# Optimization experiments

Measured on AMD Instinct MI355X. Metric: run time of the kernel, lower is better.

Reference implementation:

```python
import jax, jax.numpy as jnp
import numpy as np

B, N, L, K, C1 = 128, 300, 600, 19, 100  # batch, num_cnns, input_length, filter_size, fc hidden
PS = 7  # pool size == stride
LC = L - (K - 1)               # 582, conv output length
LP = (LC - PS) // PS + 1       # 83, pooled length
NC = 2                         # num_classes
EPS = 1e-5


def _bn(x, g, b, m, v):
    # eval-mode batchnorm, params broadcast along given axes already
    return g * (x - m) * jax.lax.rsqrt(v + EPS) + b


def setup_inputs() -> dict:
    key = jax.random.key(0)
    ks = jax.random.split(key, 20)
    f = lambda i, shape, s=0.1: (jax.random.normal(ks[i], shape, dtype=jnp.float32) * s)
    pv = lambda i, shape: (jax.random.uniform(ks[i], shape, dtype=jnp.float32) + 0.5)
    return {
        'x': jax.random.normal(ks[0], (B, 4, L), dtype=jnp.float32),
        'conv_w': f(1, (N, 4, K)), 'conv_b': f(2, (N,)),
        'bn1_g': pv(3, (N,)), 'bn1_b': f(4, (N,)), 'bn1_m': f(5, (N,)), 'bn1_v': pv(6, (N,)),
        'fc1_w': f(7, (N, C1, LP)), 'fc1_b': f(8, (N, C1)),
        'bn2_g': pv(9, (N, C1)), 'bn2_b': f(10, (N, C1)), 'bn2_m': f(11, (N, C1)), 'bn2_v': pv(12, (N, C1)),
        'fc2_w': f(13, (N, C1)), 'fc2_b': f(14, (N,)),
        'bn3_g': pv(15, (N,)), 'bn3_b': f(16, (N,)), 'bn3_m': f(17, (N,)), 'bn3_v': pv(18, (N,)),
        'final_w': f(19, (NC, N)), 'final_b': jnp.zeros((NC,), dtype=jnp.float32),
    }


def reference(x, conv_w, conv_b, bn1_g, bn1_b, bn1_m, bn1_v,
              fc1_w, fc1_b, bn2_g, bn2_b, bn2_m, bn2_v,
              fc2_w, fc2_b, bn3_g, bn3_b, bn3_m, bn3_v,
              final_w, final_b):
    # grouped conv on a repeated input == plain conv with 4 in-channels, N out-channels
    h = jax.lax.conv_general_dilated(x, conv_w, window_strides=(1,), padding='VALID',
                                     dimension_numbers=('NCH', 'OIH', 'NCH'))  # [B,N,582]
    h = h + conv_b[None, :, None]
    h = _bn(h, bn1_g[None, :, None], bn1_b[None, :, None], bn1_m[None, :, None], bn1_v[None, :, None])
    h = jnp.exp(h)
    # MaxPool1d(7,7): [B,N,582] -> [B,N,83]
    h = jax.lax.reduce_window(h, -jnp.inf, jax.lax.max,
                              window_dimensions=(1, 1, PS), window_strides=(1, 1, PS), padding='VALID')
    # grouped 1x1 conv == per-unit dense: [B,N,83] x [N,100,83] -> [B,N,100]
    h = jnp.einsum('bnp,nhp->bnh', h, fc1_w) + fc1_b[None]
    h = jax.nn.relu(_bn(h, bn2_g[None], bn2_b[None], bn2_m[None], bn2_v[None]))
    # second grouped 1x1 conv: [B,N,100] x [N,100] -> [B,N]
    h = jnp.einsum('bnh,nh->bn', h, fc2_w) + fc2_b[None]
    h = jax.nn.relu(_bn(h, bn3_g[None], bn3_b[None], bn3_m[None], bn3_v[None]))
    return h @ final_w.T + final_b  # [B,num_classes]
```

## Files before the change

kernel.cpp:

```cpp
#include <hip/hip_runtime.h>
#include <math.h>

#define EPS_ 1e-5f

__global__ __launch_bounds__(256) void kP(const float* __restrict__ conv_w,
                                          float* __restrict__ cw4) {
    const int cq = blockIdx.x;
    const int c  = cq / 5;
    const int kq = cq - c * 5;
    for (int n = threadIdx.x; n < 300; n += 256) {
        float4 v;
        const int k0 = 4 * kq;
        v.x = (k0 + 0 < 19) ? conv_w[n * 76 + c * 19 + k0 + 0] : 0.f;
        v.y = (k0 + 1 < 19) ? conv_w[n * 76 + c * 19 + k0 + 1] : 0.f;
        v.z = (k0 + 2 < 19) ? conv_w[n * 76 + c * 19 + k0 + 2] : 0.f;
        v.w = (k0 + 3 < 19) ? conv_w[n * 76 + c * 19 + k0 + 3] : 0.f;
        reinterpret_cast<float4*>(cw4)[(c * 5 + kq) * 300 + n] = v;
    }
}

__global__ __launch_bounds__(64) void kA(
        const float* __restrict__ x,
        const float* __restrict__ cw4,
        const float* __restrict__ conv_b,
        const float* __restrict__ g1, const float* __restrict__ b1,
        const float* __restrict__ m1, const float* __restrict__ v1,
        float* __restrict__ pooled)
{
    const int id  = blockIdx.x;
    const int b   = id / 112;
    const int sub = id - b * 112;
    if (sub >= 105) return;
    const int ng  = sub / 21;
    const int pc  = sub - ng * 21;
    const int p0c = pc * 4;
    const int p0  = (p0c > 79) ? 79 : p0c;
    const int lane = threadIdx.x;
    const int n   = ng * 64 + lane;
    const int nc  = (n < 300) ? n : 299;

    const float4* w4 = reinterpret_cast<const float4*>(cw4);

    float acc[28];
    #pragma unroll
    for (int i = 0; i < 28; ++i) acc[i] = 0.f;

    #pragma unroll 1
    for (int c = 0; c < 4; ++c) {
        const float* xc = x + b * 2400 + c * 600 + 7 * p0;
        float xw[46];
        #pragma unroll
        for (int j = 0; j < 46; ++j) xw[j] = xc[j];
        #pragma unroll
        for (int kq = 0; kq < 5; ++kq) {
            const float4 wv = w4[(c * 5 + kq) * 300 + nc];
            const int ni = (kq == 4) ? 3 : 4;
            #pragma unroll
            for (int i = 0; i < ni; ++i) {
                const int k = 4 * kq + i;
                const float wvv = (i == 0) ? wv.x : (i == 1) ? wv.y
                                : (i == 2) ? wv.z : wv.w;
                #pragma unroll
                for (int p = 0; p < 4; ++p)
                    #pragma unroll
                    for (int q = 0; q < 7; ++q)
                        acc[p * 7 + q] = fmaf(xw[7 * p + q + k], wvv,
                                              acc[p * 7 + q]);
            }
        }
    }

    const float A1 = g1[nc] * rsqrtf(v1[nc] + EPS_);
    const float B1 = fmaf(A1, conv_b[nc] - m1[nc], b1[nc]);
    if (n < 300) {
        float* op = pooled + ((size_t)n * 83 + p0) * 128 + b;
        #pragma unroll
        for (int p = 0; p < 4; ++p) {
            float mx = -INFINITY;
            #pragma unroll
            for (int q = 0; q < 7; ++q)
                mx = fmaxf(mx, fmaf(A1, acc[p * 7 + q], B1));
            op[p * 128] = __expf(mx);
        }
    }
}

__global__ __launch_bounds__(256) void kB(
        const float* __restrict__ pooled,
        const float* __restrict__ fc1w,
        const float* __restrict__ fc1b,
        const float* __restrict__ g2, const float* __restrict__ b2,
        const float* __restrict__ m2, const float* __restrict__ v2,
        const float* __restrict__ fc2w,
        float* __restrict__ sp)
{
    __shared__ float sW[83 * 60];
    __shared__ float sRed[4][64];
    const int id  = blockIdx.x;
    const int n   = id >> 2;
    const int rem = id & 3;
    const int bh  = rem >> 1;
    const int hq  = rem & 1;
    const int tid = threadIdx.x;

    {
        const float* src = fc1w + (size_t)n * 8300 + hq * 50 * 83;
        for (int i = tid; i < 4150; i += 256) {
            const int h = i / 83, p = i - h * 83;
            sW[p * 60 + h] = src[i];
        }
        for (int i = tid; i < 830; i += 256) {
            const int p = i / 10, h = 50 + (i - p * 10);
            sW[p * 60 + h] = 0.f;
        }
    }
    __syncthreads();

    const int lane = tid & 63;
    const int wv   = __builtin_amdgcn_readfirstlane(tid >> 6);
    const int h0   = wv * 13;
    const int nh   = (wv < 3) ? 13 : 11;
    const int bb   = bh * 64 + lane;

    const float* pp = pooled + (size_t)n * 83 * 128 + bb;

    float acc[13];
    #pragma unroll
    for (int j = 0; j < 13; ++j) acc[j] = 0.f;

    #pragma unroll 4
    for (int p = 0; p < 83; ++p) {
        const float pv = pp[p * 128];
        const float* wrow = sW + p * 60 + h0;
        #pragma unroll
        for (int j = 0; j < 13; ++j)
            acc[j] = fmaf(wrow[j], pv, acc[j]);
    }

    const int hbase = n * 100 + hq * 50 + h0;
    float part = 0.f;
    for (int j = 0; j < nh; ++j) {
        const int hi = hbase + j;
        const float A2 = g2[hi] * rsqrtf(v2[hi] + EPS_);
        const float C2 = fmaf(A2, fc1b[hi] - m2[hi], b2[hi]);
        part = fmaf(fmaxf(fmaf(A2, acc[j], C2), 0.f), fc2w[hi], part);
    }
    sRed[wv][lane] = part;
    __syncthreads();

    if (tid < 64) {
        const float s = sRed[0][tid] + sRed[1][tid] + sRed[2][tid] + sRed[3][tid];
        sp[((size_t)hq * 300 + n) * 128 + bh * 64 + tid] = s;
    }
}

__global__ __launch_bounds__(64) void kC(
        const float* __restrict__ sp,
        const float* __restrict__ fc2b,
        const float* __restrict__ g3, const float* __restrict__ b3,
        const float* __restrict__ m3, const float* __restrict__ v3,
        const float* __restrict__ fw,
        const float* __restrict__ fb,
        float* __restrict__ out)
{
    const int b = blockIdx.x, t = threadIdx.x;
    float a0 = 0.f, a1 = 0.f;
    for (int nn = t; nn < 300; nn += 64) {
        const float s = sp[nn * 128 + b] + sp[(300 + nn) * 128 + b] + fc2b[nn];
        const float A3 = g3[nn] * rsqrtf(v3[nn] + EPS_);
        const float z = fmaxf(fmaf(A3, s - m3[nn], b3[nn]), 0.f);
        a0 = fmaf(z, fw[nn], a0);
        a1 = fmaf(z, fw[300 + nn], a1);
    }
    #pragma unroll
    for (int off = 32; off > 0; off >>= 1) {
        a0 += __shfl_xor(a0, off, 64);
        a1 += __shfl_xor(a1, off, 64);
    }
    if (t == 0) {
        out[b * 2 + 0] = a0 + fb[0];
        out[b * 2 + 1] = a1 + fb[1];
    }
}

extern "C" void kernel_launch(void* const* d_in, const int* in_sizes, int n_in,
                              void* d_out, int out_size, void* d_ws, size_t ws_size,
                              hipStream_t stream) {
    const float* x      = (const float*)d_in[0];
    const float* conv_w = (const float*)d_in[1];
    const float* conv_b = (const float*)d_in[2];
    const float* g1 = (const float*)d_in[3];
    const float* b1 = (const float*)d_in[4];
    const float* m1 = (const float*)d_in[5];
    const float* v1 = (const float*)d_in[6];
    const float* fc1_w = (const float*)d_in[7];
    const float* fc1_b = (const float*)d_in[8];
    const float* g2 = (const float*)d_in[9];
    const float* b2 = (const float*)d_in[10];
    const float* m2 = (const float*)d_in[11];
    const float* v2 = (const float*)d_in[12];
    const float* fc2_w = (const float*)d_in[13];
    const float* fc2_b = (const float*)d_in[14];
    const float* g3 = (const float*)d_in[15];
    const float* b3 = (const float*)d_in[16];
    const float* m3 = (const float*)d_in[17];
    const float* v3 = (const float*)d_in[18];
    const float* fw = (const float*)d_in[19];
    const float* fb = (const float*)d_in[20];
    float* out = (float*)d_out;

    float* pooled = (float*)d_ws;
    float* sp     = pooled + (size_t)300 * 83 * 128;
    float* cw4    = sp + 76800;

    kP<<<20, 256, 0, stream>>>(conv_w, cw4);
    kA<<<128 * 112, 64, 0, stream>>>(x, cw4, conv_b, g1, b1, m1, v1, pooled);
    kB<<<1200, 256, 0, stream>>>(pooled, fc1_w, fc1_b, g2, b2, m2, v2,
                                 fc2_w, sp);
    kC<<<128, 64, 0, stream>>>(sp, fc2_b, g3, b3, m3, v3, fw, fb, out);
}
```

Baseline: 174.7 us.

## Fuse final classifier into kB via last-block atomics; pack two waves per kA block

Removes the separate kC launch. kB blocks now count completion per (unit, batch-half) with an atomic counter, and whichever half-block finishes second applies BN3, ReLU and the final linear layer, then atomically adds into the output. The output is pre-initialised with the bias and the counters are zeroed in kP. kA is also reshaped to 128-thread blocks holding two independent wavefronts, which halves the block count. The trade-off is heavy float atomic contention on 256 output values (300 adds each) and a summation order that is no longer deterministic.

```diff
diff --git a/kernel.cpp b/kernel.cpp
--- a/kernel.cpp
+++ b/kernel.cpp
@@ -4,10 +4,19 @@
 #define EPS_ 1e-5f
 
 __global__ __launch_bounds__(256) void kP(const float* __restrict__ conv_w,
-                                          float* __restrict__ cw4) {
+                                          float* __restrict__ cw4,
+                                          unsigned* __restrict__ cnt,
+                                          const float* __restrict__ fb,
+                                          float* __restrict__ out) {
     const int cq = blockIdx.x;
     const int c  = cq / 5;
     const int kq = cq - c * 5;
+    if (cq == 0) {
+        out[threadIdx.x] = fb[threadIdx.x & 1];
+    }
+    if (cq == 1) {
+        for (int i = threadIdx.x; i < 600; i += 256) cnt[i] = 0u;
+    }
     for (int n = threadIdx.x; n < 300; n += 256) {
         float4 v;
         const int k0 = 4 * kq;
@@ -19,7 +28,7 @@
     }
 }
 
-__global__ __launch_bounds__(64) void kA(
+__global__ __launch_bounds__(128) void kA(
         const float* __restrict__ x,
         const float* __restrict__ cw4,
         const float* __restrict__ conv_b,
@@ -28,14 +37,16 @@
         float* __restrict__ pooled)
 {
     const int id  = blockIdx.x;
-    const int b   = id / 112;
-    const int sub = id - b * 112;
+    const int b   = id / 56;
+    const int i2  = id - b * 56;
+    const int wv  = __builtin_amdgcn_readfirstlane(threadIdx.x >> 6);
+    const int sub = i2 * 2 + wv;
     if (sub >= 105) return;
     const int ng  = sub / 21;
     const int pc  = sub - ng * 21;
     const int p0c = pc * 4;
     const int p0  = (p0c > 79) ? 79 : p0c;
-    const int lane = threadIdx.x;
+    const int lane = threadIdx.x & 63;
     const int n   = ng * 64 + lane;
     const int nc  = (n < 300) ? n : 299;
 
@@ -53,13 +64,13 @@
         for (int j = 0; j < 46; ++j) xw[j] = xc[j];
         #pragma unroll
         for (int kq = 0; kq < 5; ++kq) {
-            const float4 wv = w4[(c * 5 + kq) * 300 + nc];
+            const float4 wv4 = w4[(c * 5 + kq) * 300 + nc];
             const int ni = (kq == 4) ? 3 : 4;
             #pragma unroll
             for (int i = 0; i < ni; ++i) {
                 const int k = 4 * kq + i;
-                const float wvv = (i == 0) ? wv.x : (i == 1) ? wv.y
-                                : (i == 2) ? wv.z : wv.w;
+                const float wvv = (i == 0) ? wv4.x : (i == 1) ? wv4.y
+                                : (i == 2) ? wv4.z : wv4.w;
                 #pragma unroll
                 for (int p = 0; p < 4; ++p)
                     #pragma unroll
@@ -92,10 +103,17 @@
         const float* __restrict__ g2, const float* __restrict__ b2,
         const float* __restrict__ m2, const float* __restrict__ v2,
         const float* __restrict__ fc2w,
-        float* __restrict__ sp)
+        float* __restrict__ sp,
+        unsigned* __restrict__ cnt,
+        const float* __restrict__ fc2b,
+        const float* __restrict__ g3, const float* __restrict__ b3,
+        const float* __restrict__ m3, const float* __restrict__ v3,
+        const float* __restrict__ fw,
+        float* __restrict__ out)
 {
     __shared__ float sW[83 * 60];
     __shared__ float sRed[4][64];
+    __shared__ unsigned sOld;
     const int id  = blockIdx.x;
     const int n   = id >> 2;
     const int rem = id & 3;
@@ -148,38 +166,24 @@
     sRed[wv][lane] = part;
     __syncthreads();
 
+    float s = 0.f;
     if (tid < 64) {
-        const float s = sRed[0][tid] + sRed[1][tid] + sRed[2][tid] + sRed[3][tid];
+        s = sRed[0][tid] + sRed[1][tid] + sRed[2][tid] + sRed[3][tid];
         sp[((size_t)hq * 300 + n) * 128 + bh * 64 + tid] = s;
     }
-}
-
-__global__ __launch_bounds__(64) void kC(
-        const float* __restrict__ sp,
-        const float* __restrict__ fc2b,
-        const float* __restrict__ g3, const float* __restrict__ b3,
-        const float* __restrict__ m3, const float* __restrict__ v3,
-        const float* __restrict__ fw,
-        const float* __restrict__ fb,
-        float* __restrict__ out)
-{
-    const int b = blockIdx.x, t = threadIdx.x;
-    float a0 = 0.f, a1 = 0.f;
-    for (int nn = t; nn < 300; nn += 64) {
-        const float s = sp[nn * 128 + b] + sp[(300 + nn) * 128 + b] + fc2b[nn];
-        const float A3 = g3[nn] * rsqrtf(v3[nn] + EPS_);
-        const float z = fmaxf(fmaf(A3, s - m3[nn], b3[nn]), 0.f);
-        a0 = fmaf(z, fw[nn], a0);
-        a1 = fmaf(z, fw[300 + nn], a1);
-    }
-    #pragma unroll
-    for (int off = 32; off > 0; off >>= 1) {
-        a0 += __shfl_xor(a0, off, 64);
-        a1 += __shfl_xor(a1, off, 64);
-    }
-    if (t == 0) {
-        out[b * 2 + 0] = a0 + fb[0];
-        out[b * 2 + 1] = a1 + fb[1];
+    __threadfence();
+    __syncthreads();
+    if (tid == 0) sOld = atomicAdd(&cnt[n * 2 + bh], 1u);
+    __syncthreads();
+    if (sOld == 1u && tid < 64) {
+        __threadfence();
+        const float sO = sp[((size_t)(hq ^ 1) * 300 + n) * 128 + bh * 64 + tid];
+        const float tot = s + sO + fc2b[n];
+        const float A3 = g3[n] * rsqrtf(v3[n] + EPS_);
+        const float z  = fmaxf(fmaf(A3, tot - m3[n], b3[n]), 0.f);
+        const int bidx = bh * 64 + tid;
+        atomicAdd(&out[bidx * 2 + 0], z * fw[n]);
+        atomicAdd(&out[bidx * 2 + 1], z * fw[300 + n]);
     }
 }
 
@@ -212,10 +216,11 @@
     float* pooled = (float*)d_ws;
     float* sp     = pooled + (size_t)300 * 83 * 128;
     float* cw4    = sp + 76800;
-
-    kP<<<20, 256, 0, stream>>>(conv_w, cw4);
-    kA<<<128 * 112, 64, 0, stream>>>(x, cw4, conv_b, g1, b1, m1, v1, pooled);
+    unsigned* cnt = (unsigned*)(cw4 + 24000);
+
+    kP<<<20, 256, 0, stream>>>(conv_w, cw4, cnt, fb, out);
+    kA<<<128 * 56, 128, 0, stream>>>(x, cw4, conv_b, g1, b1, m1, v1, pooled);
     kB<<<1200, 256, 0, stream>>>(pooled, fc1_w, fc1_b, g2, b2, m2, v2,
-                                 fc2_w, sp);
-    kC<<<128, 64, 0, stream>>>(sp, fc2_b, g3, b3, m3, v3, fw, fb, out);
-}
+                                 fc2_w, sp, cnt, fc2_b, g3, b3, m3, v3,
+                                 fw, out);
+}
```

Result: slower. 265.5 us (+52.0%).
